# Kernel tuning notes

Hardware: AMD Instinct MI355X
Metric: run time of the kernel (lower is better)

## Reference

```python
import jax, jax.numpy as jnp
import numpy as np

NEG = -9e15

def setup_inputs() -> dict:
    key = jax.random.key(0)
    k_h, k_adj, k_W, k_bW, k_a1, k_b1, k_a2, k_b2 = jax.random.split(key, 8)
    N, IN, OUT = 8192, 512, 512
    h = jax.random.normal(k_h, (N, IN), dtype=jnp.float32)
    adj = jax.random.randint(k_adj, (N, N), 0, 2, dtype=jnp.int32)
    # torch Linear default init: U(-1/sqrt(fan_in), 1/sqrt(fan_in))
    s_in = 1.0 / np.sqrt(IN)
    s_out = 1.0 / np.sqrt(OUT)
    W = jax.random.uniform(k_W, (IN, OUT), minval=-s_in, maxval=s_in, dtype=jnp.float32)
    bW = jax.random.uniform(k_bW, (OUT,), minval=-s_in, maxval=s_in, dtype=jnp.float32)
    a1 = jax.random.uniform(k_a1, (OUT,), minval=-s_out, maxval=s_out, dtype=jnp.float32)
    b1 = jax.random.uniform(k_b1, (), minval=-s_out, maxval=s_out, dtype=jnp.float32)
    a2 = jax.random.uniform(k_a2, (OUT,), minval=-s_out, maxval=s_out, dtype=jnp.float32)
    b2 = jax.random.uniform(k_b2, (), minval=-s_out, maxval=s_out, dtype=jnp.float32)
    return {"h": h, "adj": adj, "W": W, "bW": bW, "a1": a1, "b1": b1, "a2": a2, "b2": b2}

def reference(h, adj, W, bW, a1, b1, a2, b2):
    alpha = 0.2
    # Wh: [N, OUT]; dropout is identity at inference (training=False)
    Wh = h @ W + bW
    Wha1 = Wh @ a1 + b1  # [N]
    Wha2 = Wh @ a2 + b2  # [N]
    e = Wha1[:, None] + Wha2[None, :]  # [N, N] broadcast additive scores
    e = jnp.where(e > 0, e, alpha * e)  # leaky relu
    e = jnp.where(adj > 0, e, jnp.float32(-9e15))
    attention = jax.nn.softmax(e, axis=1)
    h_prime = attention @ Wh  # [N, OUT]
    return h_prime
```

## Files before the change

kernel.cpp:

```cpp
#include <hip/hip_runtime.h>
#include <stdint.h>


#define NN 8192
#define DD 512

typedef __attribute__((ext_vector_type(8))) short short8;
typedef __attribute__((ext_vector_type(4))) float f32x4;
typedef __attribute__((ext_vector_type(4))) float float4v;
typedef __attribute__((ext_vector_type(4))) unsigned short ushort4v;

__device__ __forceinline__ uint16_t f2bf(float f) {
  union { float f; uint32_t u; } v; v.f = f;
  uint32_t u = v.u;
  u += 0x7fffu + ((u >> 16) & 1u);
  return (uint16_t)(u >> 16);
}
__device__ __forceinline__ float bf2f(uint16_t b) {
  union { uint32_t u; float f; } v; v.u = ((uint32_t)b) << 16;
  return v.f;
}

__device__ __forceinline__ void async_copy16(uint16_t* lds, const uint16_t* g) {
  __builtin_amdgcn_global_load_lds(
      (const __attribute__((address_space(1))) uint32_t*)g,
      (__attribute__((address_space(3))) uint32_t*)lds, 16, 0, 0);
}

__global__ __launch_bounds__(256) void conv_wt(const float* __restrict__ W,
                                               uint16_t* __restrict__ WT) {
  __shared__ float ts[64][65];
  int tid = threadIdx.x;
  int kt = (blockIdx.x >> 3) * 64, ct = (blockIdx.x & 7) * 64;
  #pragma unroll
  for (int it = 0; it < 4; ++it) {
    int idx = it * 256 + tid;
    int r = idx >> 4, q = idx & 15;
    float4v v = *(const float4v*)(W + (size_t)(kt + r) * 512 + ct + q * 4);
    ts[r][q * 4 + 0] = v.x; ts[r][q * 4 + 1] = v.y;
    ts[r][q * 4 + 2] = v.z; ts[r][q * 4 + 3] = v.w;
  }
  __syncthreads();
  #pragma unroll
  for (int it = 0; it < 4; ++it) {
    int idx = it * 256 + tid;
    int c = idx >> 4, q = idx & 15;
    ushort4v p;
    p.x = f2bf(ts[q * 4 + 0][c]); p.y = f2bf(ts[q * 4 + 1][c]);
    p.z = f2bf(ts[q * 4 + 2][c]); p.w = f2bf(ts[q * 4 + 3][c]);
    *(ushort4v*)(WT + (size_t)(ct + c) * 512 + kt + q * 4) = p;
  }
}

__global__ __launch_bounds__(512) void wh_gemm(const float* __restrict__ h,
                                               const uint16_t* __restrict__ WT,
                                               const float* __restrict__ bW,
                                               const float* __restrict__ a1,
                                               const float* __restrict__ a2,
                                               uint16_t* __restrict__ WhT,
                                               float* __restrict__ s1g,
                                               float* __restrict__ s2g) {
  __shared__ __align__(16) uint16_t At[32 * 32];
  __shared__ __align__(16) uint16_t Bt[512 * 32];
  __shared__ float s1loc[32], s2loc[32];
  int tid = threadIdx.x;
  int wave = tid >> 6, lane = tid & 63;
  int l15 = lane & 15, quad = lane >> 4;
  int i0 = blockIdx.x * 32;
  if (tid < 32) { s1loc[tid] = 0.f; s2loc[tid] = 0.f; }
  f32x4 acc[2][4] = {};
  for (int k0 = 0; k0 < 512; k0 += 32) {
    if (tid < 256) {
      int r = tid >> 3, ks = (tid & 7) * 4;
      float4v hv = *(const float4v*)(h + (size_t)(i0 + r) * 512 + k0 + ks);
      ushort4v p;
      p.x = f2bf(hv.x); p.y = f2bf(hv.y); p.z = f2bf(hv.z); p.w = f2bf(hv.w);
      *(ushort4v*)&At[r * 32 + ks] = p;
    }
    #pragma unroll
    for (int rr = 0; rr < 4; ++rr) {
      int idx = rr * 512 + tid;
      int c = idx >> 2, q = idx & 3;
      async_copy16(&Bt[idx * 8], WT + c * 512 + k0 + q * 8);
    }
    __syncthreads();
    short8 a0 = *(const short8*)&At[l15 * 32 + quad * 8];
    short8 a1f = *(const short8*)&At[(l15 + 16) * 32 + quad * 8];
    #pragma unroll
    for (int nt = 0; nt < 4; ++nt) {
      int c = wave * 64 + nt * 16 + l15;
      short8 b = *(const short8*)&Bt[c * 32 + quad * 8];
      acc[0][nt] = __builtin_amdgcn_mfma_f32_16x16x32_bf16(a0, b, acc[0][nt], 0, 0, 0);
      acc[1][nt] = __builtin_amdgcn_mfma_f32_16x16x32_bf16(a1f, b, acc[1][nt], 0, 0, 0);
    }
    __syncthreads();
  }
  #pragma unroll
  for (int mt = 0; mt < 2; ++mt) {
    int ib = i0 + mt * 16 + quad * 4;
    float r1[4] = {0.f, 0.f, 0.f, 0.f};
    float r2[4] = {0.f, 0.f, 0.f, 0.f};
    #pragma unroll
    for (int nt = 0; nt < 4; ++nt) {
      int c = wave * 64 + nt * 16 + l15;
      float bias = bW[c];
      float a1c = a1[c], a2c = a2[c];
      float v0 = acc[mt][nt].x + bias;
      float v1 = acc[mt][nt].y + bias;
      float v2 = acc[mt][nt].z + bias;
      float v3 = acc[mt][nt].w + bias;
      ushort4v p;
      p.x = f2bf(v0); p.y = f2bf(v1); p.z = f2bf(v2); p.w = f2bf(v3);
      *(ushort4v*)&WhT[(size_t)c * 8192 + ib] = p;
      r1[0] = fmaf(v0, a1c, r1[0]); r1[1] = fmaf(v1, a1c, r1[1]);
      r1[2] = fmaf(v2, a1c, r1[2]); r1[3] = fmaf(v3, a1c, r1[3]);
      r2[0] = fmaf(v0, a2c, r2[0]); r2[1] = fmaf(v1, a2c, r2[1]);
      r2[2] = fmaf(v2, a2c, r2[2]); r2[3] = fmaf(v3, a2c, r2[3]);
    }
    #pragma unroll
    for (int v = 0; v < 4; ++v) {
      int row = mt * 16 + quad * 4 + v;
      atomicAdd(&s1loc[row], r1[v]);
      atomicAdd(&s2loc[row], r2[v]);
    }
  }
  __syncthreads();
  if (tid < 32) {
    s1g[i0 + tid] = s1loc[tid];
    s2g[i0 + tid] = s2loc[tid];
  }
}

__global__ __launch_bounds__(256) void w_k(const int* __restrict__ adj,
                                           const float* __restrict__ s1,
                                           const float* __restrict__ s2,
                                           const float* __restrict__ b1,
                                           const float* __restrict__ b2,
                                           uint16_t* __restrict__ w,
                                           float* __restrict__ dinv) {
  __shared__ float wsum[4];
  int i = blockIdx.x;
  int tid = threadIdx.x;
  float base = s1[i] + b1[0] + b2[0];
  const int* arow = adj + (size_t)i * 8192;
  uint16_t* wrow = w + (size_t)i * 8192;
  float sum = 0.f;
  #pragma unroll
  for (int it = 0; it < 8; ++it) {
    int j = it * 1024 + tid * 4;
    int4 av = *(const int4*)(arow + j);
    float4v sv = *(const float4v*)(s2 + j);
    float e, wv;
    ushort4v p;
    e = base + sv.x; e = fmaxf(e, 0.2f * e);
    wv = (av.x > 0) ? __expf(e) : 0.f; p.x = f2bf(wv); sum += bf2f(p.x);
    e = base + sv.y; e = fmaxf(e, 0.2f * e);
    wv = (av.y > 0) ? __expf(e) : 0.f; p.y = f2bf(wv); sum += bf2f(p.y);
    e = base + sv.z; e = fmaxf(e, 0.2f * e);
    wv = (av.z > 0) ? __expf(e) : 0.f; p.z = f2bf(wv); sum += bf2f(p.z);
    e = base + sv.w; e = fmaxf(e, 0.2f * e);
    wv = (av.w > 0) ? __expf(e) : 0.f; p.w = f2bf(wv); sum += bf2f(p.w);
    *(ushort4v*)(wrow + j) = p;
  }
  #pragma unroll
  for (int o = 32; o > 0; o >>= 1) sum += __shfl_down(sum, o);
  if ((tid & 63) == 0) wsum[tid >> 6] = sum;
  __syncthreads();
  if (tid == 0) dinv[i] = 1.0f / (wsum[0] + wsum[1] + wsum[2] + wsum[3]);
}

__global__ __launch_bounds__(512, 4) void pv_gemm(const uint16_t* __restrict__ w,
                                                  const uint16_t* __restrict__ WhT,
                                                  const float* __restrict__ dinv,
                                                  float* __restrict__ out) {
  __shared__ __align__(16) uint16_t At[64 * 128];
  __shared__ __align__(16) uint16_t Bt[128 * 128];
  __shared__ float sdv[64];
  int tid = threadIdx.x;
  int wave = tid >> 6, lane = tid & 63;
  int l15 = lane & 15, quad = lane >> 4;
  int rb = blockIdx.x & 127, cb = blockIdx.x >> 7;
  int i0 = rb * 64, c0 = cb * 128;
  if (tid < 64) sdv[tid] = dinv[i0 + tid];
  f32x4 acc[4] = {};
  for (int j0 = 0; j0 < 8192; j0 += 128) {
    #pragma unroll
    for (int it = 0; it < 2; ++it) {
      int idx = it * 512 + tid;
      int r = idx >> 4, p = idx & 15;
      int sc = p ^ (r & 15);
      async_copy16(&At[idx * 8], w + (size_t)(i0 + r) * 8192 + j0 + sc * 8);
    }
    #pragma unroll
    for (int it = 0; it < 4; ++it) {
      int idx = it * 512 + tid;
      int r = idx >> 4, p = idx & 15;
      int sc = p ^ (r & 15);
      async_copy16(&Bt[idx * 8], WhT + (size_t)(c0 + r) * 8192 + j0 + sc * 8);
    }
    __syncthreads();
    int brow = wave * 16 + l15;
    #pragma unroll
    for (int ks = 0; ks < 4; ++ks) {
      int ch = ks * 4 + quad;
      short8 b = *(const short8*)&Bt[brow * 128 + ((ch ^ (brow & 15)) * 8)];
      #pragma unroll
      for (int rt = 0; rt < 4; ++rt) {
        int arow = rt * 16 + l15;
        short8 a = *(const short8*)&At[arow * 128 + ((ch ^ (arow & 15)) * 8)];
        acc[rt] = __builtin_amdgcn_mfma_f32_16x16x32_bf16(a, b, acc[rt], 0, 0, 0);
      }
    }
    __syncthreads();
  }
  #pragma unroll
  for (int rt = 0; rt < 4; ++rt) {
    #pragma unroll
    for (int v = 0; v < 4; ++v) {
      int rloc = rt * 16 + quad * 4 + v;
      out[(size_t)(i0 + rloc) * 512 + c0 + wave * 16 + l15] = acc[rt][v] * sdv[rloc];
    }
  }
}

__global__ __launch_bounds__(512) void attn_k(const int* __restrict__ adj,
                                              const float* __restrict__ s1,
                                              const float* __restrict__ s2,
                                              const float* __restrict__ b1,
                                              const float* __restrict__ b2,
                                              const uint16_t* __restrict__ WhT,
                                              float* __restrict__ out) {
  __shared__ __align__(16) uint16_t At[32 * 32];
  __shared__ __align__(16) uint16_t Bt[512 * 32];
  __shared__ float dred[512];
  __shared__ float dinv[32];
  int tid = threadIdx.x;
  int wave = tid >> 6, lane = tid & 63;
  int l15 = lane & 15, quad = lane >> 4;
  int i0 = blockIdx.x * 32;
  int wr = tid >> 4;
  int wc = (tid & 15) * 2;
  float s1v = s1[i0 + wr] + b1[0] + b2[0];
  float dpart = 0.f;
  f32x4 acc[2][4] = {};
  const int* adjrow = adj + (size_t)(i0 + wr) * 8192 + wc;
  for (int j0 = 0; j0 < 8192; j0 += 32) {
    int2 av = *(const int2*)(adjrow + j0);
    float2 s2v = *(const float2*)(s2 + j0 + wc);
    float e0 = s1v + s2v.x; e0 = fmaxf(e0, 0.2f * e0);
    float e1 = s1v + s2v.y; e1 = fmaxf(e1, 0.2f * e1);
    float w0 = (av.x > 0) ? __expf(e0) : 0.f;
    float w1 = (av.y > 0) ? __expf(e1) : 0.f;
    dpart += w0 + w1;
    uint32_t packed = (uint32_t)f2bf(w0) | ((uint32_t)f2bf(w1) << 16);
    *(uint32_t*)&At[wr * 32 + wc] = packed;
    #pragma unroll
    for (int rr = 0; rr < 4; ++rr) {
      int idx = rr * 512 + tid;
      int c = idx >> 2, q = idx & 3;
      async_copy16(&Bt[idx * 8], WhT + (size_t)c * 8192 + j0 + q * 8);
    }
    __syncthreads();
    short8 a0 = *(const short8*)&At[l15 * 32 + quad * 8];
    short8 a1f = *(const short8*)&At[(l15 + 16) * 32 + quad * 8];
    #pragma unroll
    for (int nt = 0; nt < 4; ++nt) {
      short8 b = *(const short8*)&Bt[(wave * 64 + nt * 16 + l15) * 32 + quad * 8];
      acc[0][nt] = __builtin_amdgcn_mfma_f32_16x16x32_bf16(a0, b, acc[0][nt], 0, 0, 0);
      acc[1][nt] = __builtin_amdgcn_mfma_f32_16x16x32_bf16(a1f, b, acc[1][nt], 0, 0, 0);
    }
    __syncthreads();
  }
  dred[tid] = dpart;
  __syncthreads();
  if (tid < 32) {
    float s = 0.f;
    #pragma unroll
    for (int q = 0; q < 16; ++q) s += dred[tid * 16 + q];
    dinv[tid] = 1.0f / s;
  }
  __syncthreads();
  #pragma unroll
  for (int mt = 0; mt < 2; ++mt) {
    #pragma unroll
    for (int nt = 0; nt < 4; ++nt) {
      int c = wave * 64 + nt * 16 + l15;
      #pragma unroll
      for (int v = 0; v < 4; ++v) {
        int row = mt * 16 + quad * 4 + v;
        out[(size_t)(i0 + row) * 512 + c] = acc[mt][nt][v] * dinv[row];
      }
    }
  }
}

extern "C" void kernel_launch(void* const* d_in, const int* in_sizes, int n_in,
                              void* d_out, int out_size, void* d_ws, size_t ws_size,
                              hipStream_t stream) {
  const float* h   = (const float*)d_in[0];
  const int*   adj = (const int*)d_in[1];
  const float* W   = (const float*)d_in[2];
  const float* bW  = (const float*)d_in[3];
  const float* a1  = (const float*)d_in[4];
  const float* b1  = (const float*)d_in[5];
  const float* a2  = (const float*)d_in[6];
  const float* b2  = (const float*)d_in[7];
  float* out = (float*)d_out;
  char* ws = (char*)d_ws;

  const size_t NEED = 143228928ULL;
  if (ws_size >= NEED) {
    uint16_t* w   = (uint16_t*)(ws);
    uint16_t* WhT = (uint16_t*)(ws + 134217728);
    uint16_t* WT  = (uint16_t*)(ws + 142606336);
    float* s1     = (float*)(ws + 143130624);
    float* s2     = (float*)(ws + 143163392);
    float* dinv   = (float*)(ws + 143196160);

    conv_wt<<<64, 256, 0, stream>>>(W, WT);
    wh_gemm<<<256, 512, 0, stream>>>(h, WT, bW, a1, a2, WhT, s1, s2);
    w_k<<<8192, 256, 0, stream>>>(adj, s1, s2, b1, b2, w, dinv);
    pv_gemm<<<512, 512, 0, stream>>>(w, WhT, dinv, out);
  } else {
    uint16_t* WhT = (uint16_t*)(ws);
    uint16_t* WT  = (uint16_t*)(ws + 8388608);
    float* s1     = (float*)(ws + 8912896);
    float* s2     = (float*)(ws + 8945664);

    conv_wt<<<64, 256, 0, stream>>>(W, WT);
    wh_gemm<<<256, 512, 0, stream>>>(h, WT, bW, a1, a2, WhT, s1, s2);
    attn_k<<<256, 512, 0, stream>>>(adj, s1, s2, b1, b2, WhT, out);
  }
}
```

Baseline: 537.8 us.

## Fuse attention-weight computation into PV GEMM, dropping materialized weight matrix

Replaces the separate w_k kernel, which wrote a bf16 NxN weight matrix, and the pv_gemm that read it back, with one fused kernel. Each block computes exp(leaky_relu) weights from adj on the fly into LDS and accumulates row sums for the normalization. This removes the 128MB weight write and read. The cost is that adj (int32, 256MB) is now re-read by each of the 4 column blocks instead of once, and the exp work is repeated 4 times, with adj loads done synchronously rather than through async copies.

```diff
diff --git a/kernel.cpp b/kernel.cpp
--- a/kernel.cpp
+++ b/kernel.cpp
@@ -6,6 +6,7 @@
 #define DD 512
 
 typedef __attribute__((ext_vector_type(8))) short short8;
+typedef __attribute__((ext_vector_type(8))) unsigned short ushort8;
 typedef __attribute__((ext_vector_type(4))) float f32x4;
 typedef __attribute__((ext_vector_type(4))) float float4v;
 typedef __attribute__((ext_vector_type(4))) unsigned short ushort4v;
@@ -131,48 +132,18 @@
   }
 }
 
-__global__ __launch_bounds__(256) void w_k(const int* __restrict__ adj,
-                                           const float* __restrict__ s1,
-                                           const float* __restrict__ s2,
-                                           const float* __restrict__ b1,
-                                           const float* __restrict__ b2,
-                                           uint16_t* __restrict__ w,
-                                           float* __restrict__ dinv) {
-  __shared__ float wsum[4];
-  int i = blockIdx.x;
-  int tid = threadIdx.x;
-  float base = s1[i] + b1[0] + b2[0];
-  const int* arow = adj + (size_t)i * 8192;
-  uint16_t* wrow = w + (size_t)i * 8192;
-  float sum = 0.f;
-  #pragma unroll
-  for (int it = 0; it < 8; ++it) {
-    int j = it * 1024 + tid * 4;
-    int4 av = *(const int4*)(arow + j);
-    float4v sv = *(const float4v*)(s2 + j);
-    float e, wv;
-    ushort4v p;
-    e = base + sv.x; e = fmaxf(e, 0.2f * e);
-    wv = (av.x > 0) ? __expf(e) : 0.f; p.x = f2bf(wv); sum += bf2f(p.x);
-    e = base + sv.y; e = fmaxf(e, 0.2f * e);
-    wv = (av.y > 0) ? __expf(e) : 0.f; p.y = f2bf(wv); sum += bf2f(p.y);
-    e = base + sv.z; e = fmaxf(e, 0.2f * e);
-    wv = (av.z > 0) ? __expf(e) : 0.f; p.z = f2bf(wv); sum += bf2f(p.z);
-    e = base + sv.w; e = fmaxf(e, 0.2f * e);
-    wv = (av.w > 0) ? __expf(e) : 0.f; p.w = f2bf(wv); sum += bf2f(p.w);
-    *(ushort4v*)(wrow + j) = p;
-  }
-  #pragma unroll
-  for (int o = 32; o > 0; o >>= 1) sum += __shfl_down(sum, o);
-  if ((tid & 63) == 0) wsum[tid >> 6] = sum;
-  __syncthreads();
-  if (tid == 0) dinv[i] = 1.0f / (wsum[0] + wsum[1] + wsum[2] + wsum[3]);
-}
-
-__global__ __launch_bounds__(512, 4) void pv_gemm(const uint16_t* __restrict__ w,
-                                                  const uint16_t* __restrict__ WhT,
-                                                  const float* __restrict__ dinv,
-                                                  float* __restrict__ out) {
+#define WCOMP(dstv, slot, aval, sval, basev, rs)                    \
+  { float e_ = (basev) + (sval); e_ = fmaxf(e_, 0.2f * e_);         \
+    float wv_ = ((aval) > 0) ? __expf(e_) : 0.f;                    \
+    uint16_t u_ = f2bf(wv_); (dstv)[slot] = u_; (rs) += bf2f(u_); }
+
+__global__ __launch_bounds__(512, 4) void fused_attn(const int* __restrict__ adj,
+                                                     const float* __restrict__ s1,
+                                                     const float* __restrict__ s2,
+                                                     const float* __restrict__ b1,
+                                                     const float* __restrict__ b2,
+                                                     const uint16_t* __restrict__ WhT,
+                                                     float* __restrict__ out) {
   __shared__ __align__(16) uint16_t At[64 * 128];
   __shared__ __align__(16) uint16_t Bt[128 * 128];
   __shared__ float sdv[64];
@@ -181,23 +152,50 @@
   int l15 = lane & 15, quad = lane >> 4;
   int rb = blockIdx.x & 127, cb = blockIdx.x >> 7;
   int i0 = rb * 64, c0 = cb * 128;
-  if (tid < 64) sdv[tid] = dinv[i0 + tid];
+  int r0 = tid >> 4, pp = tid & 15;
+  int sc = pp ^ (r0 & 15);
+  const int* arow0 = adj + (size_t)(i0 + r0) * NN + sc * 8;
+  const int* arow1 = arow0 + (size_t)32 * NN;
+  float bias = b1[0] + b2[0];
+  float base0 = s1[i0 + r0] + bias;
+  float base1 = s1[i0 + r0 + 32] + bias;
+  float rsum0 = 0.f, rsum1 = 0.f;
+  uint16_t* at0 = &At[(r0 * 16 + pp) * 8];
+  uint16_t* at1 = &At[((r0 + 32) * 16 + pp) * 8];
   f32x4 acc[4] = {};
-  for (int j0 = 0; j0 < 8192; j0 += 128) {
-    #pragma unroll
-    for (int it = 0; it < 2; ++it) {
-      int idx = it * 512 + tid;
-      int r = idx >> 4, p = idx & 15;
-      int sc = p ^ (r & 15);
-      async_copy16(&At[idx * 8], w + (size_t)(i0 + r) * 8192 + j0 + sc * 8);
-    }
+  for (int j0 = 0; j0 < NN; j0 += 128) {
+    int4 a00 = *(const int4*)(arow0 + j0);
+    int4 a01 = *(const int4*)(arow0 + j0 + 4);
+    int4 a10 = *(const int4*)(arow1 + j0);
+    int4 a11 = *(const int4*)(arow1 + j0 + 4);
+    float4v sv0 = *(const float4v*)(s2 + j0 + sc * 8);
+    float4v sv1 = *(const float4v*)(s2 + j0 + sc * 8 + 4);
     #pragma unroll
     for (int it = 0; it < 4; ++it) {
       int idx = it * 512 + tid;
-      int r = idx >> 4, p = idx & 15;
-      int sc = p ^ (r & 15);
-      async_copy16(&Bt[idx * 8], WhT + (size_t)(c0 + r) * 8192 + j0 + sc * 8);
-    }
+      int r = idx >> 4, q = idx & 15;
+      int bsc = q ^ (r & 15);
+      async_copy16(&Bt[idx * 8], WhT + (size_t)(c0 + r) * NN + j0 + bsc * 8);
+    }
+    ushort8 w0, w1;
+    WCOMP(w0, 0, a00.x, sv0.x, base0, rsum0);
+    WCOMP(w0, 1, a00.y, sv0.y, base0, rsum0);
+    WCOMP(w0, 2, a00.z, sv0.z, base0, rsum0);
+    WCOMP(w0, 3, a00.w, sv0.w, base0, rsum0);
+    WCOMP(w0, 4, a01.x, sv1.x, base0, rsum0);
+    WCOMP(w0, 5, a01.y, sv1.y, base0, rsum0);
+    WCOMP(w0, 6, a01.z, sv1.z, base0, rsum0);
+    WCOMP(w0, 7, a01.w, sv1.w, base0, rsum0);
+    WCOMP(w1, 0, a10.x, sv0.x, base1, rsum1);
+    WCOMP(w1, 1, a10.y, sv0.y, base1, rsum1);
+    WCOMP(w1, 2, a10.z, sv0.z, base1, rsum1);
+    WCOMP(w1, 3, a10.w, sv0.w, base1, rsum1);
+    WCOMP(w1, 4, a11.x, sv1.x, base1, rsum1);
+    WCOMP(w1, 5, a11.y, sv1.y, base1, rsum1);
+    WCOMP(w1, 6, a11.z, sv1.z, base1, rsum1);
+    WCOMP(w1, 7, a11.w, sv1.w, base1, rsum1);
+    *(ushort8*)at0 = w0;
+    *(ushort8*)at1 = w1;
     __syncthreads();
     int brow = wave * 16 + l15;
     #pragma unroll
@@ -206,90 +204,29 @@
       short8 b = *(const short8*)&Bt[brow * 128 + ((ch ^ (brow & 15)) * 8)];
       #pragma unroll
       for (int rt = 0; rt < 4; ++rt) {
-        int arow = rt * 16 + l15;
-        short8 a = *(const short8*)&At[arow * 128 + ((ch ^ (arow & 15)) * 8)];
+        int ar = rt * 16 + l15;
+        short8 a = *(const short8*)&At[ar * 128 + ((ch ^ (ar & 15)) * 8)];
         acc[rt] = __builtin_amdgcn_mfma_f32_16x16x32_bf16(a, b, acc[rt], 0, 0, 0);
       }
     }
     __syncthreads();
   }
   #pragma unroll
+  for (int o = 1; o < 16; o <<= 1) {
+    rsum0 += __shfl_xor(rsum0, o);
+    rsum1 += __shfl_xor(rsum1, o);
+  }
+  if (pp == 0) {
+    sdv[r0] = 1.0f / rsum0;
+    sdv[r0 + 32] = 1.0f / rsum1;
+  }
+  __syncthreads();
+  #pragma unroll
   for (int rt = 0; rt < 4; ++rt) {
     #pragma unroll
     for (int v = 0; v < 4; ++v) {
       int rloc = rt * 16 + quad * 4 + v;
-      out[(size_t)(i0 + rloc) * 512 + c0 + wave * 16 + l15] = acc[rt][v] * sdv[rloc];
-    }
-  }
-}
-
-__global__ __launch_bounds__(512) void attn_k(const int* __restrict__ adj,
-                                              const float* __restrict__ s1,
-                                              const float* __restrict__ s2,
-                                              const float* __restrict__ b1,
-                                              const float* __restrict__ b2,
-                                              const uint16_t* __restrict__ WhT,
-                                              float* __restrict__ out) {
-  __shared__ __align__(16) uint16_t At[32 * 32];
-  __shared__ __align__(16) uint16_t Bt[512 * 32];
-  __shared__ float dred[512];
-  __shared__ float dinv[32];
-  int tid = threadIdx.x;
-  int wave = tid >> 6, lane = tid & 63;
-  int l15 = lane & 15, quad = lane >> 4;
-  int i0 = blockIdx.x * 32;
-  int wr = tid >> 4;
-  int wc = (tid & 15) * 2;
-  float s1v = s1[i0 + wr] + b1[0] + b2[0];
-  float dpart = 0.f;
-  f32x4 acc[2][4] = {};
-  const int* adjrow = adj + (size_t)(i0 + wr) * 8192 + wc;
-  for (int j0 = 0; j0 < 8192; j0 += 32) {
-    int2 av = *(const int2*)(adjrow + j0);
-    float2 s2v = *(const float2*)(s2 + j0 + wc);
-    float e0 = s1v + s2v.x; e0 = fmaxf(e0, 0.2f * e0);
-    float e1 = s1v + s2v.y; e1 = fmaxf(e1, 0.2f * e1);
-    float w0 = (av.x > 0) ? __expf(e0) : 0.f;
-    float w1 = (av.y > 0) ? __expf(e1) : 0.f;
-    dpart += w0 + w1;
-    uint32_t packed = (uint32_t)f2bf(w0) | ((uint32_t)f2bf(w1) << 16);
-    *(uint32_t*)&At[wr * 32 + wc] = packed;
-    #pragma unroll
-    for (int rr = 0; rr < 4; ++rr) {
-      int idx = rr * 512 + tid;
-      int c = idx >> 2, q = idx & 3;
-      async_copy16(&Bt[idx * 8], WhT + (size_t)c * 8192 + j0 + q * 8);
-    }
-    __syncthreads();
-    short8 a0 = *(const short8*)&At[l15 * 32 + quad * 8];
-    short8 a1f = *(const short8*)&At[(l15 + 16) * 32 + quad * 8];
-    #pragma unroll
-    for (int nt = 0; nt < 4; ++nt) {
-      short8 b = *(const short8*)&Bt[(wave * 64 + nt * 16 + l15) * 32 + quad * 8];
-      acc[0][nt] = __builtin_amdgcn_mfma_f32_16x16x32_bf16(a0, b, acc[0][nt], 0, 0, 0);
-      acc[1][nt] = __builtin_amdgcn_mfma_f32_16x16x32_bf16(a1f, b, acc[1][nt], 0, 0, 0);
-    }
-    __syncthreads();
-  }
-  dred[tid] = dpart;
-  __syncthreads();
-  if (tid < 32) {
-    float s = 0.f;
-    #pragma unroll
-    for (int q = 0; q < 16; ++q) s += dred[tid * 16 + q];
-    dinv[tid] = 1.0f / s;
-  }
-  __syncthreads();
-  #pragma unroll
-  for (int mt = 0; mt < 2; ++mt) {
-    #pragma unroll
-    for (int nt = 0; nt < 4; ++nt) {
-      int c = wave * 64 + nt * 16 + l15;
-      #pragma unroll
-      for (int v = 0; v < 4; ++v) {
-        int row = mt * 16 + quad * 4 + v;
-        out[(size_t)(i0 + row) * 512 + c] = acc[mt][nt][v] * dinv[row];
-      }
+      out[(size_t)(i0 + rloc) * DD + c0 + wave * 16 + l15] = acc[rt][v] * sdv[rloc];
     }
   }
 }
@@ -308,27 +245,12 @@
   float* out = (float*)d_out;
   char* ws = (char*)d_ws;
 
-  const size_t NEED = 143228928ULL;
-  if (ws_size >= NEED) {
-    uint16_t* w   = (uint16_t*)(ws);
-    uint16_t* WhT = (uint16_t*)(ws + 134217728);
-    uint16_t* WT  = (uint16_t*)(ws + 142606336);
-    float* s1     = (float*)(ws + 143130624);
-    float* s2     = (float*)(ws + 143163392);
-    float* dinv   = (float*)(ws + 143196160);
-
-    conv_wt<<<64, 256, 0, stream>>>(W, WT);
-    wh_gemm<<<256, 512, 0, stream>>>(h, WT, bW, a1, a2, WhT, s1, s2);
-    w_k<<<8192, 256, 0, stream>>>(adj, s1, s2, b1, b2, w, dinv);
-    pv_gemm<<<512, 512, 0, stream>>>(w, WhT, dinv, out);
-  } else {
-    uint16_t* WhT = (uint16_t*)(ws);
-    uint16_t* WT  = (uint16_t*)(ws + 8388608);
-    float* s1     = (float*)(ws + 8912896);
-    float* s2     = (float*)(ws + 8945664);
-
-    conv_wt<<<64, 256, 0, stream>>>(W, WT);
-    wh_gemm<<<256, 512, 0, stream>>>(h, WT, bW, a1, a2, WhT, s1, s2);
-    attn_k<<<256, 512, 0, stream>>>(adj, s1, s2, b1, b2, WhT, out);
-  }
-}
+  uint16_t* WhT = (uint16_t*)(ws);
+  uint16_t* WT  = (uint16_t*)(ws + 8388608);
+  float* s1     = (float*)(ws + 8912896);
+  float* s2     = (float*)(ws + 8945664);
+
+  conv_wt<<<64, 256, 0, stream>>>(W, WT);
+  wh_gemm<<<256, 512, 0, stream>>>(h, WT, bW, a1, a2, WhT, s1, s2);
+  fused_attn<<<512, 512, 0, stream>>>(adj, s1, s2, b1, b2, WhT, out);
+}
```

After: 501.8 us. 6.7% less time.
